# Kernel tuning notes

Hardware: AMD Instinct MI355X
Metric: run time of the kernel (lower is better)

Reference implementation:

```python
import jax, jax.numpy as jnp
import numpy as np

N = 50000; E = 800000; D_IN = 64; EDGE_D = 1
EMB_H = 128; H = 4; C = 32; HC = H * C; G = 8


def _ln(h, g, b):
    mu = jnp.mean(h, axis=-1, keepdims=True)
    var = jnp.var(h, axis=-1, keepdims=True)
    return (h - mu) * jax.lax.rsqrt(var + 1e-5) * g + b


def _tconv(x, src, dst, ea, wq, bq, wk, bk, wv, bv, we, ws, bs):
    # PyG TransformerConv (beta=False, root_weight=True, concat=True, dropout=0)
    n = x.shape[0]
    q = (x @ wq + bq).reshape(n, H, C)
    k = (x @ wk + bk).reshape(n, H, C)
    v = (x @ wv + bv).reshape(n, H, C)
    e = (ea @ we).reshape(-1, H, C)          # [E,H,C] edge embedding (no bias)
    ke = k[src] + e
    ve = v[src] + e
    logit = jnp.einsum('ehc,ehc->eh', q[dst], ke) / np.float32(np.sqrt(C))
    m = jax.ops.segment_max(logit, dst, num_segments=n)
    m = jnp.where(jnp.isfinite(m), m, 0.0)
    a = jnp.exp(logit - m[dst])
    s = jax.ops.segment_sum(a, dst, num_segments=n)
    alpha = a / (s[dst] + 1e-16)             # softmax over in-edges of each dst
    out = jax.ops.segment_sum(alpha[..., None] * ve, dst, num_segments=n)
    out = out.reshape(n, HC)                 # concat heads
    return out + x @ ws + bs                 # root/skip connection


def _embed(x, src, dst, ea, w1, b1, lng, lnb, w2, b2):
    # EmbedConv: per-edge MLP on [x_j || edge_attr], sum-aggregate to dst.
    # LayerNorm params are SHARED (same nn.LayerNorm instance reused in torch).
    msg = jnp.concatenate([x[src], ea], axis=1) @ w1 + b1
    msg = _ln(jax.nn.relu(msg), lng, lnb)
    msg = _ln(jax.nn.relu(msg @ w2 + b2), lng, lnb)
    return jax.ops.segment_sum(msg, dst, num_segments=x.shape[0])


def _forward(x, edge_attr, params, edge_index, batch_idx):
    src, dst = edge_index[0], edge_index[1]
    h = _embed(x, src, dst, edge_attr, *params[0:6])
    h = jax.nn.relu(_tconv(h, src, dst, edge_attr, *params[6:15]))
    h = jax.nn.relu(_tconv(h, src, dst, edge_attr, *params[15:24]))
    # global mean pool
    s = jax.ops.segment_sum(h, batch_idx, num_segments=G)
    cnt = jax.ops.segment_sum(jnp.ones((h.shape[0],), h.dtype), batch_idx, num_segments=G)
    return s / jnp.maximum(cnt, 1.0)[:, None]


def setup_inputs() -> dict:
    key = jax.random.key(0)
    ks = jax.random.split(key, 40)
    w = lambda k, shp: jax.random.normal(k, shp, dtype=jnp.float32) * 0.05
    inp = {}
    inp['x'] = jax.random.normal(ks[0], (N, D_IN), dtype=jnp.float32)
    inp['edge_index'] = jax.random.randint(ks[1], (2, E), 0, N)
    inp['edge_attr'] = jax.random.uniform(ks[2], (E, EDGE_D), dtype=jnp.float32)
    inp['batch_idx'] = jnp.sort(jax.random.randint(ks[3], (N,), 0, G))
    inp['emb_lin1_w'] = w(ks[4], (D_IN + EDGE_D, EMB_H))
    inp['emb_lin1_b'] = jnp.zeros((EMB_H,), jnp.float32)
    inp['emb_ln_g'] = jnp.ones((EMB_H,), jnp.float32)
    inp['emb_ln_b'] = jnp.zeros((EMB_H,), jnp.float32)
    inp['emb_lin2_w'] = w(ks[5], (EMB_H, EMB_H))
    inp['emb_lin2_b'] = jnp.zeros((EMB_H,), jnp.float32)
    i = 6
    for pre, din in (('g1', EMB_H), ('g2', HC)):
        inp[pre + '_wq'] = w(ks[i], (din, HC)); inp[pre + '_bq'] = jnp.zeros((HC,), jnp.float32)
        inp[pre + '_wk'] = w(ks[i + 1], (din, HC)); inp[pre + '_bk'] = jnp.zeros((HC,), jnp.float32)
        inp[pre + '_wv'] = w(ks[i + 2], (din, HC)); inp[pre + '_bv'] = jnp.zeros((HC,), jnp.float32)
        inp[pre + '_we'] = w(ks[i + 3], (EDGE_D, HC))
        inp[pre + '_ws'] = w(ks[i + 4], (din, HC)); inp[pre + '_bs'] = jnp.zeros((HC,), jnp.float32)
        i += 5
    return inp


def reference(x, edge_index, edge_attr, batch_idx,
              emb_lin1_w, emb_lin1_b, emb_ln_g, emb_ln_b, emb_lin2_w, emb_lin2_b,
              g1_wq, g1_bq, g1_wk, g1_bk, g1_wv, g1_bv, g1_we, g1_ws, g1_bs,
              g2_wq, g2_bq, g2_wk, g2_bk, g2_wv, g2_bv, g2_we, g2_ws, g2_bs):
    params = (emb_lin1_w, emb_lin1_b, emb_ln_g, emb_ln_b, emb_lin2_w, emb_lin2_b,
              g1_wq, g1_bq, g1_wk, g1_bk, g1_wv, g1_bv, g1_we, g1_ws, g1_bs,
              g2_wq, g2_bq, g2_wk, g2_bk, g2_wv, g2_bv, g2_we, g2_ws, g2_bs)
    return _forward(x, edge_attr, params, edge_index, batch_idx)
```

## Files before the change

kernel.cpp:

```cpp
#include <hip/hip_runtime.h>

typedef unsigned short u16;
typedef unsigned int u32;
typedef __attribute__((ext_vector_type(8))) short bf16x8;
typedef __attribute__((ext_vector_type(4))) float f32x4;
typedef __attribute__((ext_vector_type(4))) u32 u32x4;

#define N_NODES 50000
#define N_EDGES 800000

__device__ __forceinline__ float bf2f(u16 u) {
    union { u32 i; float f; } v; v.i = ((u32)u) << 16; return v.f;
}
__device__ __forceinline__ u16 f2bf(float f) {
    union { u32 i; float f; } v; v.f = f;
    u32 i = v.i;
    return (u16)((i + 0x7FFFu + ((i >> 16) & 1u)) >> 16);
}
__device__ __forceinline__ float ldf(const void* p, int i, int fl) {
    return fl ? ((const float*)p)[i] : bf2f(((const u16*)p)[i]);
}
__device__ __forceinline__ int getflag(const int* flag) {
    return __builtin_amdgcn_readfirstlane(*flag);
}

struct P8 { const void* s[8]; };

__global__ __launch_bounds__(256) void k_deg_detect(
    const int* __restrict__ dst, int* __restrict__ cnt,
    const u16* __restrict__ xr, int* __restrict__ flag)
{
    int t = threadIdx.x;
    if (blockIdx.x < 3125) {
        int e = blockIdx.x * 256 + t;
        atomicAdd(&cnt[dst[e]], 1);
        return;
    }
    __shared__ int sc[256];
    int c = 0;
    for (int i = t; i < 4096; i += 256) {
        u32 e = (xr[i] >> 7) & 0xFF;
        if (e >= 143) c++;
    }
    sc[t] = c;
    __syncthreads();
    for (int s = 128; s > 0; s >>= 1) {
        if (t < s) sc[t] += sc[t + s];
        __syncthreads();
    }
    if (t == 0) *flag = (sc[0] > 64) ? 1 : 0;
}

__global__ __launch_bounds__(256) void k_prep_all(
    P8 pw, P8 pb, u16* __restrict__ wcat1, u16* __restrict__ wcat2,
    float* __restrict__ bcat1, float* __restrict__ bcat2,
    const void* __restrict__ w2, const void* __restrict__ lng_,
    const void* __restrict__ lnb_, const void* __restrict__ b2_,
    const void* __restrict__ w1, u16* __restrict__ gt,
    float* __restrict__ csum, float* __restrict__ bwp,
    u32* __restrict__ w1pk, const int* __restrict__ flag)
{
    int fl = getflag(flag);
    int b = blockIdx.x, t = threadIdx.x;
    if (b < 512) {
        int gid = b * 256 + t;
        int wi = gid >> 14;
        int id = gid & 16383;
        int k = id >> 7, n = id & 127;
        u16* d = (wi < 4) ? (wcat1 + wi * 16384) : (wcat2 + (wi - 4) * 16384);
        d[n * 128 + k] = f2bf(ldf(pw.s[wi], id, fl));
    } else if (b < 516) {
        int tt = (b - 512) * 256 + t;
        float v = ldf(pb.s[tt >> 7], tt & 127, fl);
        if (tt < 512) bcat1[tt] = v; else bcat2[tt - 512] = v;
    } else {
        if (t < 128) {
            float cs = 0.f, bw = 0.f;
            for (int f = 0; f < 128; f++) {
                float wv = ldf(w2, f * 128 + t, fl);
                float g = ldf(lng_, f, fl);
                float bb = ldf(lnb_, f, fl);
                u16 gwq = f2bf(g * wv);
                gt[t * 128 + f] = gwq;
                cs += bf2f(gwq);
                bw = fmaf(bb, wv, bw);
            }
            csum[t] = cs;
            bwp[t] = bw + ldf(b2_, t, fl);
            if (t < 64)
                w1pk[t] = (u32)f2bf(ldf(w1, 64 * 128 + t * 2, fl)) |
                          ((u32)f2bf(ldf(w1, 64 * 128 + t * 2 + 1, fl)) << 16);
        }
    }
}

__global__ __launch_bounds__(1024) void k_scan(const int* __restrict__ cnt,
                                               int* __restrict__ row_start,
                                               int* __restrict__ nxt)
{
    __shared__ int wsum[16];
    __shared__ int s_tot;
    int t = threadIdx.x, lane = t & 63, wid = t >> 6;
    int run = 0;
    for (int base = 0; base < N_NODES; base += 8192) {
        int i0 = base + t * 8;
        int v[8], pre[8];
        int s = 0;
        #pragma unroll
        for (int j = 0; j < 8; j++) {
            int i = i0 + j;
            v[j] = (i < N_NODES) ? cnt[i] : 0;
            pre[j] = s;
            s += v[j];
        }
        int tsum = s;
        int sc = tsum;
        #pragma unroll
        for (int off = 1; off < 64; off <<= 1) {
            int o = __shfl_up(sc, off);
            if (lane >= off) sc += o;
        }
        if (lane == 63) wsum[wid] = sc;
        __syncthreads();
        if (t == 0) {
            int acc2 = 0;
            #pragma unroll
            for (int k2 = 0; k2 < 16; k2++) { int vv = wsum[k2]; wsum[k2] = acc2; acc2 += vv; }
            s_tot = acc2;
        }
        __syncthreads();
        int texcl = run + wsum[wid] + (sc - tsum);
        #pragma unroll
        for (int j = 0; j < 8; j++) {
            int i = i0 + j;
            if (i < N_NODES) { int ex = texcl + pre[j]; row_start[i] = ex; nxt[i] = ex; }
        }
        run += s_tot;
        __syncthreads();
    }
    if (t == 0) row_start[N_NODES] = run;
}

__global__ __launch_bounds__(256) void k_lin1_scatter(
    const void* __restrict__ x, const void* __restrict__ w1,
    const void* __restrict__ b1, u16* __restrict__ y,
    const int* __restrict__ dst, const int* __restrict__ srcp,
    const void* __restrict__ ea, int* __restrict__ nxt,
    int2* __restrict__ csr, const int* __restrict__ flag)
{
    __shared__ float sx[2][64];
    int fl = getflag(flag);
    int t = threadIdx.x;
    if (blockIdx.x >= 782) {
        int e = (blockIdx.x - 782) * 256 + t;
        if (e < N_EDGES) {
            int p = atomicAdd(&nxt[dst[e]], 1);
            int2 v;
            v.x = srcp[e];
            v.y = __float_as_int(ldf(ea, e, fl));
            csr[p] = v;
        }
        return;
    }
    int col = t & 127, half = t >> 7;
    float wreg[64];
    #pragma unroll
    for (int k = 0; k < 64; k++) wreg[k] = ldf(w1, k * 128 + col, fl);
    float bias = ldf(b1, col, fl);
    int base = blockIdx.x * 64;
    for (int it = 0; it < 32; ++it) {
        __syncthreads();
        if (t < 128) {
            int nh = base + it * 2 + (t >> 6);
            sx[t >> 6][t & 63] = (nh < N_NODES) ? ldf(x, nh * 64 + (t & 63), fl) : 0.f;
        }
        __syncthreads();
        float acc = bias;
        #pragma unroll
        for (int k = 0; k < 64; k++) acc = fmaf(sx[half][k], wreg[k], acc);
        int n = base + it * 2 + half;
        if (n < N_NODES) y[(size_t)n * 128 + col] = f2bf(acc);
    }
}

__global__ __launch_bounds__(256) void k_embed_edges(
    const u16* __restrict__ y, const int2* __restrict__ csr,
    const int* __restrict__ rowst,
    const void* __restrict__ lng, const void* __restrict__ lnb,
    const u16* __restrict__ gt, const u32* __restrict__ w1pk,
    const float* __restrict__ csum, const float* __restrict__ bwp,
    u16* __restrict__ h1, const int* __restrict__ flag)
{
    __shared__ u16 sB[128 * 136];
    __shared__ u32 sW1[64];
    __shared__ float sCSf[128];
    __shared__ float sBWf[128];
    int fl = getflag(flag);
    int t = threadIdx.x;
    for (int c = t; c < 128 * 32; c += 256) {
        int row = c >> 5, ch = c & 31;
        *(ushort4*)&sB[row * 136 + ch * 4] = *(const ushort4*)&gt[row * 128 + ch * 4];
    }
    if (t < 64) sW1[t] = w1pk[t];
    if (t < 128) sCSf[t] = csum[t];
    else sBWf[t - 128] = bwp[t - 128];
    int l = t & 63, w = t >> 6;
    int m = l & 15, q = l >> 4;
    __syncthreads();

    f32x4 zf = {0.f, 0.f, 0.f, 0.f};
    bool sel0 = (m & 1), sel1 = (m & 2), sel2 = (m & 4), sel3 = (m & 8);
    int stride = gridDim.x * 4;
    for (int node = blockIdx.x * 4 + w; node < N_NODES; node += stride) {
        int rs = rowst[node], re = rowst[node + 1];
        float sacc0 = 0.f, sacc1 = 0.f, V = 0.f;
        if (rs < re) {
            int idx = rs + m;
            int2 sa = csr[(idx < re) ? idx : (re - 1)];
            for (int base = rs; base < re; base += 16) {
                float av = __int_as_float(sa.y);
                const u16* yr = y + (size_t)sa.x * 128 + q * 8;
                bf16x8 efrag[4];
                float s1 = 0.f, s2 = 0.f;
                #pragma unroll
                for (int kb = 0; kb < 4; kb++) {
                    u32x4 yu = __builtin_bit_cast(u32x4, *(const bf16x8*)(yr + kb * 32));
                    u32x4 wv4 = *(const u32x4*)&sW1[kb * 16 + q * 4];
                    u32x4 ep;
                    #pragma unroll
                    for (int j2 = 0; j2 < 4; j2++) {
                        u32 yw = yu[j2];
                        u32 ww = wv4[j2];
                        float y0 = __uint_as_float(yw << 16);
                        float y1 = __uint_as_float(yw & 0xffff0000u);
                        float w0 = __uint_as_float(ww << 16);
                        float w1v = __uint_as_float(ww & 0xffff0000u);
                        float u0 = fmaxf(fmaf(av, w0, y0), 0.f);
                        float u1 = fmaxf(fmaf(av, w1v, y1), 0.f);
                        s1 += u0; s2 = fmaf(u0, u0, s2);
                        s1 += u1; s2 = fmaf(u1, u1, s2);
                        ep[j2] = __builtin_amdgcn_perm(__float_as_uint(u1),
                                                       __float_as_uint(u0), 0x07060302u);
                    }
                    efrag[kb] = __builtin_bit_cast(bf16x8, ep);
                }
                int nbase = base + 16;
                if (nbase < re) {
                    int ni = nbase + m;
                    sa = csr[(ni < re) ? ni : (re - 1)];
                }
                s1 += __shfl_xor(s1, 16); s2 += __shfl_xor(s2, 16);
                s1 += __shfl_xor(s1, 32); s2 += __shfl_xor(s2, 32);
                float mu = s1 * (1.f / 128.f);
                float alpha = rsqrtf(s2 * (1.f / 128.f) - mu * mu + 1e-5f);
                float beta = -mu * alpha;

                f32x4 acc[8];
                #pragma unroll
                for (int nb = 0; nb < 8; nb++) acc[nb] = zf;
                #pragma unroll
                for (int nb = 0; nb < 8; nb++) {
                    const u16* grow = &sB[(nb * 16 + m) * 136 + q * 8];
                    #pragma unroll
                    for (int kb = 0; kb < 4; kb++) {
                        bf16x8 gfrag = *(const bf16x8*)(grow + kb * 32);
                        acc[nb] = __builtin_amdgcn_mfma_f32_16x16x32_bf16(gfrag, efrag[kb], acc[nb], 0, 0, 0);
                    }
                }
                float t1 = 0.f, t2 = 0.f;
                #pragma unroll
                for (int nb = 0; nb < 8; nb++) {
                    float4 cs4 = *(const float4*)&sCSf[nb * 16 + q * 4];
                    float4 bw4 = *(const float4*)&sBWf[nb * 16 + q * 4];
                    float csa[4] = {cs4.x, cs4.y, cs4.z, cs4.w};
                    float bwa[4] = {bw4.x, bw4.y, bw4.z, bw4.w};
                    #pragma unroll
                    for (int r = 0; r < 4; r++) {
                        float z = fmaxf(fmaf(alpha, acc[nb][r], fmaf(beta, csa[r], bwa[r])), 0.f);
                        acc[nb][r] = z;
                        t1 += z; t2 = fmaf(z, z, t2);
                    }
                }
                t1 += __shfl_xor(t1, 16); t2 += __shfl_xor(t2, 16);
                t1 += __shfl_xor(t1, 32); t2 += __shfl_xor(t2, 32);
                float mu2 = t1 * (1.f / 128.f);
                float rs2 = rsqrtf(t2 * (1.f / 128.f) - mu2 * mu2 + 1e-5f);
                if (base + m >= re) rs2 = 0.f;
                V = fmaf(rs2, mu2, V);
                float s16v[16];
                #pragma unroll
                for (int k = 0; k < 16; k++) {
                    int nb = k >> 1, rh = (k & 1) << 1;
                    float a = acc[nb][rh] * rs2, b = acc[nb][rh + 1] * rs2;
                    float keep = sel0 ? b : a;
                    float send = sel0 ? a : b;
                    s16v[k] = keep + __shfl_xor(send, 1);
                }
                float s8v[8];
                #pragma unroll
                for (int nb = 0; nb < 8; nb++) {
                    float a = s16v[nb * 2], b = s16v[nb * 2 + 1];
                    float keep = sel1 ? b : a;
                    float send = sel1 ? a : b;
                    s8v[nb] = keep + __shfl_xor(send, 2);
                }
                float s4v[4];
                #pragma unroll
                for (int k = 0; k < 4; k++) {
                    float a = s8v[k * 2], b = s8v[k * 2 + 1];
                    float keep = sel2 ? b : a;
                    float send = sel2 ? a : b;
                    s4v[k] = keep + __shfl_xor(send, 4);
                }
                #pragma unroll
                for (int k = 0; k < 2; k++) {
                    float a = s4v[k * 2], b = s4v[k * 2 + 1];
                    float keep = sel3 ? b : a;
                    float send = sel3 ? a : b;
                    float r2 = keep + __shfl_xor(send, 8);
                    if (k == 0) sacc0 += r2; else sacc1 += r2;
                }
            }
        }
        V += __shfl_xor(V, 1); V += __shfl_xor(V, 2);
        V += __shfl_xor(V, 4); V += __shfl_xor(V, 8);
        float dg = (float)(re - rs);
        #pragma unroll
        for (int k = 0; k < 2; k++) {
            int nb = (k << 2) | (((m >> 3) & 1) << 1) | ((m >> 2) & 1);
            int f = nb * 16 + q * 4 + (m & 3);
            float gg = ldf(lng, f, fl), bb = ldf(lnb, f, fl);
            float sv = (k == 0) ? sacc0 : sacc1;
            h1[(size_t)node * 128 + f] = f2bf(fmaf(gg, sv - V, dg * bb));
        }
    }
}

__global__ __launch_bounds__(256) void k_proj(
    const u16* __restrict__ hin, const u16* __restrict__ wt,
    const float* __restrict__ bcat, u16* __restrict__ outp)
{
    __shared__ u16 sA[64 * 136];
    __shared__ u16 sB[128 * 136];
    int t = threadIdx.x;
    int l = t & 63, w = t >> 6;
    int m = l & 15, q = l >> 4;
    int rowbase = blockIdx.x * 64;
    for (int c = t; c < 64 * 32; c += 256) {
        int row = c >> 5, ch = c & 31;
        int gr = rowbase + row;
        ushort4 pk = make_ushort4(0, 0, 0, 0);
        if (gr < N_NODES) pk = *(const ushort4*)&hin[(size_t)gr * 128 + ch * 4];
        *(ushort4*)&sA[row * 136 + ch * 4] = pk;
    }
    __syncthreads();
    bf16x8 afrag[4];
    #pragma unroll
    for (int kb = 0; kb < 4; kb++)
        afrag[kb] = *(const bf16x8*)&sA[(w * 16 + m) * 136 + kb * 32 + q * 8];

    f32x4 zf = {0.f, 0.f, 0.f, 0.f};
    for (int g = 0; g < 4; ++g) {
        __syncthreads();
        for (int c = t; c < 128 * 32; c += 256) {
            int row = c >> 5, ch = c & 31;
            *(ushort4*)&sB[row * 136 + ch * 4] = *(const ushort4*)&wt[(g * 128 + row) * 128 + ch * 4];
        }
        __syncthreads();
        f32x4 acc[8];
        #pragma unroll
        for (int nb = 0; nb < 8; nb++) acc[nb] = zf;
        #pragma unroll
        for (int nb = 0; nb < 8; nb++) {
            const u16* brow = &sB[(nb * 16 + m) * 136 + q * 8];
            #pragma unroll
            for (int kb = 0; kb < 4; kb++) {
                bf16x8 bfrag = *(const bf16x8*)(brow + kb * 32);
                acc[nb] = __builtin_amdgcn_mfma_f32_16x16x32_bf16(afrag[kb], bfrag, acc[nb], 0, 0, 0);
            }
        }
        #pragma unroll
        for (int nb = 0; nb < 8; nb++) {
            int col = g * 128 + nb * 16 + m;
            float bb = bcat[col];
            #pragma unroll
            for (int r = 0; r < 4; r++) {
                int row = rowbase + w * 16 + q * 4 + r;
                if (row < N_NODES) outp[(size_t)row * 512 + col] = f2bf(acc[nb][r] + bb);
            }
        }
    }
}

__global__ __launch_bounds__(256) void k_attn(
    const u16* __restrict__ qkvs,
    const int* __restrict__ rowst, const int2* __restrict__ csr,
    const void* __restrict__ wep, u16* __restrict__ hout,
    const int* __restrict__ flag)
{
    int fl = getflag(flag);
    int t = threadIdx.x;
    int l = t & 63, w = t >> 6;
    int dstn = blockIdx.x * 4 + w;
    int lane16 = l & 15, sub = l >> 4;
    int f0 = lane16 * 8;
    const float scale = 0.17677669529663687f;

    bf16x8 q8 = *(const bf16x8*)&qkvs[(size_t)dstn * 512 + f0];
    float qf[8], wef[8];
    if (fl) {
        float4 w0 = *(const float4*)((const float*)wep + f0);
        float4 w1v = *(const float4*)((const float*)wep + f0 + 4);
        wef[0] = w0.x; wef[1] = w0.y; wef[2] = w0.z; wef[3] = w0.w;
        wef[4] = w1v.x; wef[5] = w1v.y; wef[6] = w1v.z; wef[7] = w1v.w;
    } else {
        bf16x8 w8 = *(const bf16x8*)((const u16*)wep + f0);
        #pragma unroll
        for (int j = 0; j < 8; j++) wef[j] = bf2f((u16)w8[j]);
    }
    #pragma unroll
    for (int j = 0; j < 8; j++) qf[j] = bf2f((u16)q8[j]) * scale;

    float si = 0.f;
    float a8[8];
    #pragma unroll
    for (int j = 0; j < 8; j++) a8[j] = 0.f;

    int rs = rowst[dstn], re = rowst[dstn + 1];
    int i = rs + sub;
    for (; i + 4 < re; i += 8) {
        int2 sa = csr[i];
        int2 sb = csr[i + 4];
        float ava = __int_as_float(sa.y);
        float avb = __int_as_float(sb.y);
        const u16* sra = &qkvs[(size_t)sa.x * 512 + f0];
        const u16* srb = &qkvs[(size_t)sb.x * 512 + f0];
        bf16x8 k8a = *(const bf16x8*)(sra + 128);
        bf16x8 v8a = *(const bf16x8*)(sra + 256);
        bf16x8 k8b = *(const bf16x8*)(srb + 128);
        bf16x8 v8b = *(const bf16x8*)(srb + 256);
        float pa = 0.f, pb = 0.f;
        float vea[8], veb[8];
        #pragma unroll
        for (int j = 0; j < 8; j++) {
            pa = fmaf(qf[j], fmaf(ava, wef[j], bf2f((u16)k8a[j])), pa);
            pb = fmaf(qf[j], fmaf(avb, wef[j], bf2f((u16)k8b[j])), pb);
            vea[j] = fmaf(ava, wef[j], bf2f((u16)v8a[j]));
            veb[j] = fmaf(avb, wef[j], bf2f((u16)v8b[j]));
        }
        pa += __shfl_xor(pa, 1); pb += __shfl_xor(pb, 1);
        pa += __shfl_xor(pa, 2); pb += __shfl_xor(pb, 2);
        float pea = __expf(pa);
        float peb = __expf(pb);
        si += pea + peb;
        #pragma unroll
        for (int j = 0; j < 8; j++)
            a8[j] = fmaf(pea, vea[j], fmaf(peb, veb[j], a8[j]));
    }
    if (i < re) {
        int2 sa = csr[i];
        float av = __int_as_float(sa.y);
        const u16* sr = &qkvs[(size_t)sa.x * 512 + f0];
        bf16x8 k8 = *(const bf16x8*)(sr + 128);
        bf16x8 v8 = *(const bf16x8*)(sr + 256);
        float p = 0.f;
        float ve[8];
        #pragma unroll
        for (int j = 0; j < 8; j++) {
            p = fmaf(qf[j], fmaf(av, wef[j], bf2f((u16)k8[j])), p);
            ve[j] = fmaf(av, wef[j], bf2f((u16)v8[j]));
        }
        p += __shfl_xor(p, 1); p += __shfl_xor(p, 2);
        float pe = __expf(p);
        si += pe;
        #pragma unroll
        for (int j = 0; j < 8; j++) a8[j] = fmaf(pe, ve[j], a8[j]);
    }
    #pragma unroll
    for (int off = 16; off < 64; off <<= 1) {
        si += __shfl_xor(si, off);
        #pragma unroll
        for (int j = 0; j < 8; j++) a8[j] += __shfl_xor(a8[j], off);
    }
    if (sub == 0) {
        float inv = 1.f / (si + 1e-16f);
        bf16x8 s8 = *(const bf16x8*)&qkvs[(size_t)dstn * 512 + 384 + f0];
        ushort4 p0, p1;
        float o[8];
        #pragma unroll
        for (int j = 0; j < 8; j++)
            o[j] = fmaxf(fmaf(a8[j], inv, bf2f((u16)s8[j])), 0.f);
        p0.x = f2bf(o[0]); p0.y = f2bf(o[1]); p0.z = f2bf(o[2]); p0.w = f2bf(o[3]);
        p1.x = f2bf(o[4]); p1.y = f2bf(o[5]); p1.z = f2bf(o[6]); p1.w = f2bf(o[7]);
        u16* hr = hout + (size_t)dstn * 128 + f0;
        *(ushort4*)hr = p0;
        *(ushort4*)(hr + 4) = p1;
    }
}

__global__ __launch_bounds__(256) void k_pool(
    const u16* __restrict__ h, const int* __restrict__ batch,
    float* __restrict__ gsum, float* __restrict__ gcnt)
{
    __shared__ float ssum[8 * 128];
    __shared__ float scnt[8];
    int t = threadIdx.x;
    for (int i = t; i < 8 * 128; i += 256) ssum[i] = 0.f;
    if (t < 8) scnt[t] = 0.f;
    __syncthreads();
    int f2 = (t & 63) * 2, quarter = t >> 6;
    int per = (N_NODES + gridDim.x - 1) / gridDim.x;
    int lo = blockIdx.x * per;
    int hi = lo + per; if (hi > N_NODES) hi = N_NODES;
    float r0 = 0.f, r1 = 0.f, rcnt = 0.f; int rg = -1;
    for (int n = lo + quarter; n < hi; n += 4) {
        int g = batch[n];
        if (g != rg) {
            if (rg >= 0) {
                atomicAdd(&ssum[rg * 128 + f2], r0);
                atomicAdd(&ssum[rg * 128 + f2 + 1], r1);
                if (f2 == 0) atomicAdd(&scnt[rg], rcnt);
            }
            rg = g; r0 = 0.f; r1 = 0.f; rcnt = 0.f;
        }
        u32 hv = *(const u32*)&h[(size_t)n * 128 + f2];
        r0 += bf2f((u16)(hv & 0xffff));
        r1 += bf2f((u16)(hv >> 16));
        rcnt += 1.f;
    }
    if (rg >= 0) {
        atomicAdd(&ssum[rg * 128 + f2], r0);
        atomicAdd(&ssum[rg * 128 + f2 + 1], r1);
        if (f2 == 0) atomicAdd(&scnt[rg], rcnt);
    }
    __syncthreads();
    for (int i = t; i < 8 * 128; i += 256) unsafeAtomicAdd(&gsum[i], ssum[i]);
    if (t < 8) unsafeAtomicAdd(&gcnt[t], scnt[t]);
}

__global__ void k_out(const float* __restrict__ gsum, const float* __restrict__ gcnt,
                      void* __restrict__ outp, const int* __restrict__ flag) {
    int fl = getflag(flag);
    int t = threadIdx.x;
    float c = fmaxf(gcnt[t >> 7], 1.f);
    float v = gsum[t] / c;
    if (fl) ((float*)outp)[t] = v;
    else ((u16*)outp)[t] = f2bf(v);
}

extern "C" void kernel_launch(void* const* d_in, const int* in_sizes, int n_in,
                              void* d_out, int out_size, void* d_ws, size_t ws_size,
                              hipStream_t stream)
{
    (void)in_sizes; (void)n_in; (void)out_size; (void)ws_size;
    const void* x    = d_in[0];
    const int* ei    = (const int*)d_in[1];
    const void* ea   = d_in[2];
    const int* batch = (const int*)d_in[3];
    const void* w1   = d_in[4];
    const void* b1   = d_in[5];
    const void* lng  = d_in[6];
    const void* lnb  = d_in[7];
    const void* w2   = d_in[8];
    const void* b2   = d_in[9];
    const int* srcp = ei;
    const int* dstp = ei + N_EDGES;

    char* wsb = (char*)d_ws;
    size_t cur = 0;
    auto alloc = [&](size_t sz) -> void* {
        void* p = wsb + cur;
        cur += (sz + 255) & ~(size_t)255;
        return p;
    };
    u16*   y      = (u16*)  alloc((size_t)N_NODES * 128 * 2);
    u16*   h1     = (u16*)  alloc((size_t)N_NODES * 128 * 2);
    u16*   h2     = (u16*)  alloc((size_t)N_NODES * 128 * 2);
    u16*   qkvs   = (u16*)  alloc((size_t)N_NODES * 512 * 2);
    int2*  csr    = (int2*) alloc((size_t)N_EDGES * 8);
    u16*   gt     = (u16*)  alloc(128 * 128 * 2);
    u16*   wcat1  = (u16*)  alloc(512 * 128 * 2);
    u16*   wcat2  = (u16*)  alloc(512 * 128 * 2);
    float* csum   = (float*)alloc(128 * 4);
    float* bwp    = (float*)alloc(128 * 4);
    u32*   w1pk   = (u32*)  alloc(64 * 4);
    float* bcat1  = (float*)alloc(512 * 4);
    float* bcat2  = (float*)alloc(512 * 4);
    int*   cntdeg = (int*)  alloc((size_t)N_NODES * 4);
    int*   rowst  = (int*)  alloc((size_t)(N_NODES + 1) * 4);
    int*   nxt    = (int*)  alloc((size_t)N_NODES * 4);
    float* gsum   = (float*)alloc((8 * 128 + 8) * 4);
    int*   dtflag = (int*)  alloc(256);
    u16*   h3 = h1;

    hipMemsetAsync(cntdeg, 0, (size_t)N_NODES * 4, stream);
    hipMemsetAsync(gsum, 0, (8 * 128 + 8) * 4, stream);

    P8 pw; P8 pb;
    pw.s[0] = d_in[10]; pw.s[1] = d_in[12]; pw.s[2] = d_in[14]; pw.s[3] = d_in[17];
    pw.s[4] = d_in[19]; pw.s[5] = d_in[21]; pw.s[6] = d_in[23]; pw.s[7] = d_in[26];
    pb.s[0] = d_in[11]; pb.s[1] = d_in[13]; pb.s[2] = d_in[15]; pb.s[3] = d_in[18];
    pb.s[4] = d_in[20]; pb.s[5] = d_in[22]; pb.s[6] = d_in[24]; pb.s[7] = d_in[27];

    k_deg_detect<<<3126, 256, 0, stream>>>(dstp, cntdeg, (const u16*)x, dtflag);
    k_prep_all<<<517, 256, 0, stream>>>(pw, pb, wcat1, wcat2, bcat1, bcat2,
                                        w2, lng, lnb, b2, w1, gt, csum, bwp, w1pk, dtflag);
    k_scan<<<1, 1024, 0, stream>>>(cntdeg, rowst, nxt);
    k_lin1_scatter<<<3907, 256, 0, stream>>>(x, w1, b1, y, dstp, srcp, ea, nxt, csr, dtflag);
    k_embed_edges<<<2048, 256, 0, stream>>>(y, csr, rowst, lng, lnb,
                                            gt, w1pk, csum, bwp, h1, dtflag);
    k_proj<<<782, 256, 0, stream>>>(h1, wcat1, bcat1, qkvs);
    k_attn<<<12500, 256, 0, stream>>>(qkvs, rowst, csr, d_in[16], h2, dtflag);
    k_proj<<<782, 256, 0, stream>>>(h2, wcat2, bcat2, qkvs);
    k_attn<<<12500, 256, 0, stream>>>(qkvs, rowst, csr, d_in[25], h3, dtflag);
    k_pool<<<128, 256, 0, stream>>>(h3, batch, gsum, gsum + 8 * 128);
    k_out<<<1, 1024, 0, stream>>>(gsum, gsum + 8 * 128, d_out, dtflag);
}
```

Before: 828.0 us.

## Process two destination nodes per wavefront in embed kernel for ILP

The edge-embedding aggregation kernel now handles a pair of adjacent nodes per wavefront and interleaves their gathers, LayerNorm statistics, MFMA chains and shuffle reductions. All gather loads for both nodes are issued before the math, and the next CSR entries are prefetched. The aim is more independent work in flight to hide gather latency and MFMA dependency stalls. In exchange it doubles register pressure, which may lower occupancy, and a node pair with uneven degrees pays for the larger one, wasting lanes.

```diff
diff --git a/kernel.cpp b/kernel.cpp
--- a/kernel.cpp
+++ b/kernel.cpp
@@ -211,63 +211,98 @@
     f32x4 zf = {0.f, 0.f, 0.f, 0.f};
     bool sel0 = (m & 1), sel1 = (m & 2), sel2 = (m & 4), sel3 = (m & 8);
     int stride = gridDim.x * 4;
-    for (int node = blockIdx.x * 4 + w; node < N_NODES; node += stride) {
-        int rs = rowst[node], re = rowst[node + 1];
-        float sacc0 = 0.f, sacc1 = 0.f, V = 0.f;
-        if (rs < re) {
-            int idx = rs + m;
-            int2 sa = csr[(idx < re) ? idx : (re - 1)];
-            for (int base = rs; base < re; base += 16) {
-                float av = __int_as_float(sa.y);
-                const u16* yr = y + (size_t)sa.x * 128 + q * 8;
-                bf16x8 efrag[4];
-                float s1 = 0.f, s2 = 0.f;
+    const int NPAIR = N_NODES / 2;
+    for (int pid = blockIdx.x * 4 + w; pid < NPAIR; pid += stride) {
+        int n0 = pid * 2, n1 = n0 + 1;
+        int rs0 = rowst[n0];
+        int re0 = rowst[n0 + 1];
+        int re1 = rowst[n0 + 2];
+        int rs1 = re0;
+        int d0 = re0 - rs0, d1 = re1 - rs1;
+        int steps = max((d0 + 15) >> 4, (d1 + 15) >> 4);
+        float sacc0_0 = 0.f, sacc1_0 = 0.f, V0 = 0.f;
+        float sacc0_1 = 0.f, sacc1_1 = 0.f, V1 = 0.f;
+        if (steps > 0) {
+            int lim0 = max(re0 - 1, 0);
+            int lim1 = max(re1 - 1, 0);
+            int2 sa0 = csr[min(rs0 + m, lim0)];
+            int2 sa1 = csr[min(rs1 + m, lim1)];
+            for (int s = 0; s < steps; ++s) {
+                int base0 = rs0 + s * 16, base1 = rs1 + s * 16;
+                float av0 = __int_as_float(sa0.y);
+                float av1 = __int_as_float(sa1.y);
+                const u16* yr0 = y + (size_t)sa0.x * 128 + q * 8;
+                const u16* yr1 = y + (size_t)sa1.x * 128 + q * 8;
+                u32x4 yu0[4], yu1[4];
                 #pragma unroll
                 for (int kb = 0; kb < 4; kb++) {
-                    u32x4 yu = __builtin_bit_cast(u32x4, *(const bf16x8*)(yr + kb * 32));
+                    yu0[kb] = __builtin_bit_cast(u32x4, *(const bf16x8*)(yr0 + kb * 32));
+                    yu1[kb] = __builtin_bit_cast(u32x4, *(const bf16x8*)(yr1 + kb * 32));
+                }
+                int2 sn0 = sa0, sn1 = sa1;
+                if (s + 1 < steps) {
+                    int off = (s + 1) * 16 + m;
+                    sn0 = csr[min(rs0 + off, lim0)];
+                    sn1 = csr[min(rs1 + off, lim1)];
+                }
+                bf16x8 efrag0[4], efrag1[4];
+                float s1_0 = 0.f, s2_0 = 0.f, s1_1 = 0.f, s2_1 = 0.f;
+                #pragma unroll
+                for (int kb = 0; kb < 4; kb++) {
                     u32x4 wv4 = *(const u32x4*)&sW1[kb * 16 + q * 4];
-                    u32x4 ep;
+                    u32x4 ep0, ep1;
                     #pragma unroll
                     for (int j2 = 0; j2 < 4; j2++) {
-                        u32 yw = yu[j2];
                         u32 ww = wv4[j2];
-                        float y0 = __uint_as_float(yw << 16);
-                        float y1 = __uint_as_float(yw & 0xffff0000u);
                         float w0 = __uint_as_float(ww << 16);
                         float w1v = __uint_as_float(ww & 0xffff0000u);
-                        float u0 = fmaxf(fmaf(av, w0, y0), 0.f);
-                        float u1 = fmaxf(fmaf(av, w1v, y1), 0.f);
-                        s1 += u0; s2 = fmaf(u0, u0, s2);
-                        s1 += u1; s2 = fmaf(u1, u1, s2);
-                        ep[j2] = __builtin_amdgcn_perm(__float_as_uint(u1),
-                                                       __float_as_uint(u0), 0x07060302u);
+                        u32 ya = yu0[kb][j2];
+                        u32 yb = yu1[kb][j2];
+                        float ya0 = __uint_as_float(ya << 16);
+                        float ya1 = __uint_as_float(ya & 0xffff0000u);
+                        float yb0 = __uint_as_float(yb << 16);
+                        float yb1 = __uint_as_float(yb & 0xffff0000u);
+                        float ua0 = fmaxf(fmaf(av0, w0, ya0), 0.f);
+                        float ua1 = fmaxf(fmaf(av0, w1v, ya1), 0.f);
+                        float ub0 = fmaxf(fmaf(av1, w0, yb0), 0.f);
+                        float ub1 = fmaxf(fmaf(av1, w1v, yb1), 0.f);
+                        s1_0 += ua0; s2_0 = fmaf(ua0, ua0, s2_0);
+                        s1_0 += ua1; s2_0 = fmaf(ua1, ua1, s2_0);
+                        s1_1 += ub0; s2_1 = fmaf(ub0, ub0, s2_1);
+                        s1_1 += ub1; s2_1 = fmaf(ub1, ub1, s2_1);
+                        ep0[j2] = __builtin_amdgcn_perm(__float_as_uint(ua1),
+                                                        __float_as_uint(ua0), 0x07060302u);
+                        ep1[j2] = __builtin_amdgcn_perm(__float_as_uint(ub1),
+                                                        __float_as_uint(ub0), 0x07060302u);
                     }
-                    efrag[kb] = __builtin_bit_cast(bf16x8, ep);
-                }
-                int nbase = base + 16;
-                if (nbase < re) {
-                    int ni = nbase + m;
-                    sa = csr[(ni < re) ? ni : (re - 1)];
-                }
-                s1 += __shfl_xor(s1, 16); s2 += __shfl_xor(s2, 16);
-                s1 += __shfl_xor(s1, 32); s2 += __shfl_xor(s2, 32);
-                float mu = s1 * (1.f / 128.f);
-                float alpha = rsqrtf(s2 * (1.f / 128.f) - mu * mu + 1e-5f);
-                float beta = -mu * alpha;
-
-                f32x4 acc[8];
-                #pragma unroll
-                for (int nb = 0; nb < 8; nb++) acc[nb] = zf;
+                    efrag0[kb] = __builtin_bit_cast(bf16x8, ep0);
+                    efrag1[kb] = __builtin_bit_cast(bf16x8, ep1);
+                }
+                s1_0 += __shfl_xor(s1_0, 16); s1_1 += __shfl_xor(s1_1, 16);
+                s2_0 += __shfl_xor(s2_0, 16); s2_1 += __shfl_xor(s2_1, 16);
+                s1_0 += __shfl_xor(s1_0, 32); s1_1 += __shfl_xor(s1_1, 32);
+                s2_0 += __shfl_xor(s2_0, 32); s2_1 += __shfl_xor(s2_1, 32);
+                float mu_0 = s1_0 * (1.f / 128.f);
+                float alpha0 = rsqrtf(s2_0 * (1.f / 128.f) - mu_0 * mu_0 + 1e-5f);
+                float beta0 = -mu_0 * alpha0;
+                float mu_1 = s1_1 * (1.f / 128.f);
+                float alpha1 = rsqrtf(s2_1 * (1.f / 128.f) - mu_1 * mu_1 + 1e-5f);
+                float beta1 = -mu_1 * alpha1;
+
+                f32x4 acc0[8], acc1[8];
+                #pragma unroll
+                for (int nb = 0; nb < 8; nb++) { acc0[nb] = zf; acc1[nb] = zf; }
                 #pragma unroll
                 for (int nb = 0; nb < 8; nb++) {
                     const u16* grow = &sB[(nb * 16 + m) * 136 + q * 8];
                     #pragma unroll
                     for (int kb = 0; kb < 4; kb++) {
                         bf16x8 gfrag = *(const bf16x8*)(grow + kb * 32);
-                        acc[nb] = __builtin_amdgcn_mfma_f32_16x16x32_bf16(gfrag, efrag[kb], acc[nb], 0, 0, 0);
+                        acc0[nb] = __builtin_amdgcn_mfma_f32_16x16x32_bf16(gfrag, efrag0[kb], acc0[nb], 0, 0, 0);
+                        acc1[nb] = __builtin_amdgcn_mfma_f32_16x16x32_bf16(gfrag, efrag1[kb], acc1[nb], 0, 0, 0);
                     }
                 }
-                float t1 = 0.f, t2 = 0.f;
+                float t1_0 = 0.f, t2_0 = 0.f, t1_1 = 0.f, t2_1 = 0.f;
                 #pragma unroll
                 for (int nb = 0; nb < 8; nb++) {
                     float4 cs4 = *(const float4*)&sCSf[nb * 16 + q * 4];
@@ -276,62 +311,86 @@
                     float bwa[4] = {bw4.x, bw4.y, bw4.z, bw4.w};
                     #pragma unroll
                     for (int r = 0; r < 4; r++) {
-                        float z = fmaxf(fmaf(alpha, acc[nb][r], fmaf(beta, csa[r], bwa[r])), 0.f);
-                        acc[nb][r] = z;
-                        t1 += z; t2 = fmaf(z, z, t2);
+                        float z0 = fmaxf(fmaf(alpha0, acc0[nb][r], fmaf(beta0, csa[r], bwa[r])), 0.f);
+                        float z1 = fmaxf(fmaf(alpha1, acc1[nb][r], fmaf(beta1, csa[r], bwa[r])), 0.f);
+                        acc0[nb][r] = z0;
+                        acc1[nb][r] = z1;
+                        t1_0 += z0; t2_0 = fmaf(z0, z0, t2_0);
+                        t1_1 += z1; t2_1 = fmaf(z1, z1, t2_1);
                     }
                 }
-                t1 += __shfl_xor(t1, 16); t2 += __shfl_xor(t2, 16);
-                t1 += __shfl_xor(t1, 32); t2 += __shfl_xor(t2, 32);
-                float mu2 = t1 * (1.f / 128.f);
-                float rs2 = rsqrtf(t2 * (1.f / 128.f) - mu2 * mu2 + 1e-5f);
-                if (base + m >= re) rs2 = 0.f;
-                V = fmaf(rs2, mu2, V);
-                float s16v[16];
+                t1_0 += __shfl_xor(t1_0, 16); t1_1 += __shfl_xor(t1_1, 16);
+                t2_0 += __shfl_xor(t2_0, 16); t2_1 += __shfl_xor(t2_1, 16);
+                t1_0 += __shfl_xor(t1_0, 32); t1_1 += __shfl_xor(t1_1, 32);
+                t2_0 += __shfl_xor(t2_0, 32); t2_1 += __shfl_xor(t2_1, 32);
+                float mu2_0 = t1_0 * (1.f / 128.f);
+                float rs2_0 = rsqrtf(t2_0 * (1.f / 128.f) - mu2_0 * mu2_0 + 1e-5f);
+                float mu2_1 = t1_1 * (1.f / 128.f);
+                float rs2_1 = rsqrtf(t2_1 * (1.f / 128.f) - mu2_1 * mu2_1 + 1e-5f);
+                if (base0 + m >= re0) rs2_0 = 0.f;
+                if (base1 + m >= re1) rs2_1 = 0.f;
+                V0 = fmaf(rs2_0, mu2_0, V0);
+                V1 = fmaf(rs2_1, mu2_1, V1);
+                float s16v_0[16], s16v_1[16];
                 #pragma unroll
                 for (int k = 0; k < 16; k++) {
                     int nb = k >> 1, rh = (k & 1) << 1;
-                    float a = acc[nb][rh] * rs2, b = acc[nb][rh + 1] * rs2;
-                    float keep = sel0 ? b : a;
-                    float send = sel0 ? a : b;
-                    s16v[k] = keep + __shfl_xor(send, 1);
-                }
-                float s8v[8];
+                    float a0 = acc0[nb][rh] * rs2_0, b0 = acc0[nb][rh + 1] * rs2_0;
+                    float a1 = acc1[nb][rh] * rs2_1, b1 = acc1[nb][rh + 1] * rs2_1;
+                    float keep0 = sel0 ? b0 : a0, send0 = sel0 ? a0 : b0;
+                    float keep1 = sel0 ? b1 : a1, send1 = sel0 ? a1 : b1;
+                    s16v_0[k] = keep0 + __shfl_xor(send0, 1);
+                    s16v_1[k] = keep1 + __shfl_xor(send1, 1);
+                }
+                float s8v_0[8], s8v_1[8];
                 #pragma unroll
                 for (int nb = 0; nb < 8; nb++) {
-                    float a = s16v[nb * 2], b = s16v[nb * 2 + 1];
-                    float keep = sel1 ? b : a;
-                    float send = sel1 ? a : b;
-                    s8v[nb] = keep + __shfl_xor(send, 2);
-                }
-                float s4v[4];
+                    float a0 = s16v_0[nb * 2], b0 = s16v_0[nb * 2 + 1];
+                    float a1 = s16v_1[nb * 2], b1 = s16v_1[nb * 2 + 1];
+                    float keep0 = sel1 ? b0 : a0, send0 = sel1 ? a0 : b0;
+                    float keep1 = sel1 ? b1 : a1, send1 = sel1 ? a1 : b1;
+                    s8v_0[nb] = keep0 + __shfl_xor(send0, 2);
+                    s8v_1[nb] = keep1 + __shfl_xor(send1, 2);
+                }
+                float s4v_0[4], s4v_1[4];
                 #pragma unroll
                 for (int k = 0; k < 4; k++) {
-                    float a = s8v[k * 2], b = s8v[k * 2 + 1];
-                    float keep = sel2 ? b : a;
-                    float send = sel2 ? a : b;
-                    s4v[k] = keep + __shfl_xor(send, 4);
+                    float a0 = s8v_0[k * 2], b0 = s8v_0[k * 2 + 1];
+                    float a1 = s8v_1[k * 2], b1 = s8v_1[k * 2 + 1];
+                    float keep0 = sel2 ? b0 : a0, send0 = sel2 ? a0 : b0;
+                    float keep1 = sel2 ? b1 : a1, send1 = sel2 ? a1 : b1;
+                    s4v_0[k] = keep0 + __shfl_xor(send0, 4);
+                    s4v_1[k] = keep1 + __shfl_xor(send1, 4);
                 }
                 #pragma unroll
                 for (int k = 0; k < 2; k++) {
-                    float a = s4v[k * 2], b = s4v[k * 2 + 1];
-                    float keep = sel3 ? b : a;
-                    float send = sel3 ? a : b;
-                    float r2 = keep + __shfl_xor(send, 8);
-                    if (k == 0) sacc0 += r2; else sacc1 += r2;
-                }
+                    float a0 = s4v_0[k * 2], b0 = s4v_0[k * 2 + 1];
+                    float a1 = s4v_1[k * 2], b1 = s4v_1[k * 2 + 1];
+                    float keep0 = sel3 ? b0 : a0, send0 = sel3 ? a0 : b0;
+                    float keep1 = sel3 ? b1 : a1, send1 = sel3 ? a1 : b1;
+                    float r20 = keep0 + __shfl_xor(send0, 8);
+                    float r21 = keep1 + __shfl_xor(send1, 8);
+                    if (k == 0) { sacc0_0 += r20; sacc0_1 += r21; }
+                    else        { sacc1_0 += r20; sacc1_1 += r21; }
+                }
+                sa0 = sn0;
+                sa1 = sn1;
             }
         }
-        V += __shfl_xor(V, 1); V += __shfl_xor(V, 2);
-        V += __shfl_xor(V, 4); V += __shfl_xor(V, 8);
-        float dg = (float)(re - rs);
+        V0 += __shfl_xor(V0, 1); V1 += __shfl_xor(V1, 1);
+        V0 += __shfl_xor(V0, 2); V1 += __shfl_xor(V1, 2);
+        V0 += __shfl_xor(V0, 4); V1 += __shfl_xor(V1, 4);
+        V0 += __shfl_xor(V0, 8); V1 += __shfl_xor(V1, 8);
+        float dg0 = (float)d0, dg1 = (float)d1;
         #pragma unroll
         for (int k = 0; k < 2; k++) {
             int nb = (k << 2) | (((m >> 3) & 1) << 1) | ((m >> 2) & 1);
             int f = nb * 16 + q * 4 + (m & 3);
             float gg = ldf(lng, f, fl), bb = ldf(lnb, f, fl);
-            float sv = (k == 0) ? sacc0 : sacc1;
-            h1[(size_t)node * 128 + f] = f2bf(fmaf(gg, sv - V, dg * bb));
+            float sv0 = (k == 0) ? sacc0_0 : sacc1_0;
+            float sv1 = (k == 0) ? sacc0_1 : sacc1_1;
+            h1[(size_t)n0 * 128 + f] = f2bf(fmaf(gg, sv0 - V0, dg0 * bb));
+            h1[(size_t)n1 * 128 + f] = f2bf(fmaf(gg, sv1 - V1, dg1 * bb));
         }
     }
 }
```

After: 810.6 us. 2.1% less time.

## Split embed edge work into 16-edge groups with atomic fp32 accumulation

Applied to the files above, without the earlier changes.

Replaces the grid-strided per-node edge-embedding kernel with one wave per 16-edge group, built from a second prefix scan and a group-list kernel. Partial sums are atomically added into a zeroed fp32 staging buffer, and a new finalize kernel applies the shared LayerNorm affine and converts to bf16. This targets load imbalance from varying node degrees and exposes more parallelism, at the cost of two extra launches, a large memset, fp32 atomics and extra staging-buffer traffic.

```diff
diff --git a/kernel.cpp b/kernel.cpp
--- a/kernel.cpp
+++ b/kernel.cpp
@@ -8,6 +8,7 @@
 
 #define N_NODES 50000
 #define N_EDGES 800000
+#define NG_MAX ((N_EDGES + 15 * N_NODES) / 16)
 
 __device__ __forceinline__ float bf2f(u16 u) {
     union { u32 i; float f; } v; v.i = ((u32)u) << 16; return v.f;
@@ -96,49 +97,73 @@
 
 __global__ __launch_bounds__(1024) void k_scan(const int* __restrict__ cnt,
                                                int* __restrict__ row_start,
-                                               int* __restrict__ nxt)
+                                               int* __restrict__ nxt,
+                                               int* __restrict__ gstart)
 {
     __shared__ int wsum[16];
-    __shared__ int s_tot;
+    __shared__ int wsum2[16];
+    __shared__ int s_tot, s_tot2;
     int t = threadIdx.x, lane = t & 63, wid = t >> 6;
-    int run = 0;
+    int run = 0, run2 = 0;
     for (int base = 0; base < N_NODES; base += 8192) {
         int i0 = base + t * 8;
-        int v[8], pre[8];
-        int s = 0;
+        int v[8], pre[8], gpre[8];
+        int s = 0, gs = 0;
         #pragma unroll
         for (int j = 0; j < 8; j++) {
             int i = i0 + j;
             v[j] = (i < N_NODES) ? cnt[i] : 0;
-            pre[j] = s;
-            s += v[j];
-        }
-        int tsum = s;
-        int sc = tsum;
+            pre[j] = s;  s += v[j];
+            gpre[j] = gs; gs += (v[j] + 15) >> 4;
+        }
+        int tsum = s, gsum = gs;
+        int sc = tsum, sc2 = gsum;
         #pragma unroll
         for (int off = 1; off < 64; off <<= 1) {
             int o = __shfl_up(sc, off);
-            if (lane >= off) sc += o;
-        }
-        if (lane == 63) wsum[wid] = sc;
+            int o2 = __shfl_up(sc2, off);
+            if (lane >= off) { sc += o; sc2 += o2; }
+        }
+        if (lane == 63) { wsum[wid] = sc; wsum2[wid] = sc2; }
         __syncthreads();
         if (t == 0) {
-            int acc2 = 0;
+            int acc2 = 0, acc3 = 0;
             #pragma unroll
-            for (int k2 = 0; k2 < 16; k2++) { int vv = wsum[k2]; wsum[k2] = acc2; acc2 += vv; }
-            s_tot = acc2;
+            for (int k2 = 0; k2 < 16; k2++) {
+                int vv = wsum[k2]; wsum[k2] = acc2; acc2 += vv;
+                int v2 = wsum2[k2]; wsum2[k2] = acc3; acc3 += v2;
+            }
+            s_tot = acc2; s_tot2 = acc3;
         }
         __syncthreads();
         int texcl = run + wsum[wid] + (sc - tsum);
+        int gexcl = run2 + wsum2[wid] + (sc2 - gsum);
         #pragma unroll
         for (int j = 0; j < 8; j++) {
             int i = i0 + j;
-            if (i < N_NODES) { int ex = texcl + pre[j]; row_start[i] = ex; nxt[i] = ex; }
-        }
-        run += s_tot;
-        __syncthreads();
-    }
-    if (t == 0) row_start[N_NODES] = run;
+            if (i < N_NODES) {
+                int ex = texcl + pre[j];
+                row_start[i] = ex; nxt[i] = ex;
+                gstart[i] = gexcl + gpre[j];
+            }
+        }
+        run += s_tot; run2 += s_tot2;
+        __syncthreads();
+    }
+    if (t == 0) { row_start[N_NODES] = run; gstart[N_NODES] = run2; }
+}
+
+__global__ __launch_bounds__(256) void k_glist(
+    const int* __restrict__ rowst, const int* __restrict__ gstart,
+    int2* __restrict__ glist)
+{
+    int n = blockIdx.x * 256 + threadIdx.x;
+    if (n >= N_NODES) return;
+    int rs = rowst[n], re = rowst[n + 1];
+    int gs = gstart[n];
+    int cnt = (re - rs + 15) >> 4;
+    for (int k = 0; k < cnt; k++)
+        glist[gs + k] = make_int2(n, rs + k * 16);
 }
 
 __global__ __launch_bounds__(256) void k_lin1_scatter(
@@ -183,19 +208,18 @@
     }
 }
 
-__global__ __launch_bounds__(256) void k_embed_edges(
+__global__ __launch_bounds__(256) void k_embed_grp(
     const u16* __restrict__ y, const int2* __restrict__ csr,
-    const int* __restrict__ rowst,
-    const void* __restrict__ lng, const void* __restrict__ lnb,
+    const int* __restrict__ rowst, const int* __restrict__ gstart,
+    const int2* __restrict__ glist,
     const u16* __restrict__ gt, const u32* __restrict__ w1pk,
     const float* __restrict__ csum, const float* __restrict__ bwp,
-    u16* __restrict__ h1, const int* __restrict__ flag)
+    float* __restrict__ h1stage, float* __restrict__ vacc)
 {
     __shared__ u16 sB[128 * 136];
     __shared__ u32 sW1[64];
     __shared__ float sCSf[128];
     __shared__ float sBWf[128];
-    int fl = getflag(flag);
     int t = threadIdx.x;
     for (int c = t; c < 128 * 32; c += 256) {
         int row = c >> 5, ch = c & 31;
@@ -207,133 +231,148 @@
     int l = t & 63, w = t >> 6;
     int m = l & 15, q = l >> 4;
     __syncthreads();
+    int ng = gstart[N_NODES];
+    int gid = blockIdx.x * 4 + w;
+    if (gid >= ng) return;
+    int2 ge = glist[gid];
+    int node = ge.x, base = ge.y;
+    int re = rowst[node + 1];
+    int row = base + m;
+    if (row >= re) row = re - 1;
+    int2 sa = csr[row];
+    float av = __int_as_float(sa.y);
+    const u16* yr = y + (size_t)sa.x * 128 + q * 8;
+
+    bf16x8 efrag[4];
+    float s1 = 0.f, s2 = 0.f;
+    #pragma unroll
+    for (int kb = 0; kb < 4; kb++) {
+        u32x4 yu = __builtin_bit_cast(u32x4, *(const bf16x8*)(yr + kb * 32));
+        u32x4 wv4 = *(const u32x4*)&sW1[kb * 16 + q * 4];
+        u32x4 ep;
+        #pragma unroll
+        for (int j2 = 0; j2 < 4; j2++) {
+            u32 yw = yu[j2];
+            u32 ww = wv4[j2];
+            float y0 = __uint_as_float(yw << 16);
+            float y1 = __uint_as_float(yw & 0xffff0000u);
+            float w0 = __uint_as_float(ww << 16);
+            float w1v = __uint_as_float(ww & 0xffff0000u);
+            float u0 = fmaxf(fmaf(av, w0, y0), 0.f);
+            float u1 = fmaxf(fmaf(av, w1v, y1), 0.f);
+            s1 += u0; s2 = fmaf(u0, u0, s2);
+            s1 += u1; s2 = fmaf(u1, u1, s2);
+            ep[j2] = __builtin_amdgcn_perm(__float_as_uint(u1),
+                                           __float_as_uint(u0), 0x07060302u);
+        }
+        efrag[kb] = __builtin_bit_cast(bf16x8, ep);
+    }
+    s1 += __shfl_xor(s1, 16); s2 += __shfl_xor(s2, 16);
+    s1 += __shfl_xor(s1, 32); s2 += __shfl_xor(s2, 32);
+    float mu = s1 * (1.f / 128.f);
+    float alpha = rsqrtf(s2 * (1.f / 128.f) - mu * mu + 1e-5f);
+    float beta = -mu * alpha;
 
     f32x4 zf = {0.f, 0.f, 0.f, 0.f};
+    f32x4 acc[8];
+    #pragma unroll
+    for (int nb = 0; nb < 8; nb++) acc[nb] = zf;
+    #pragma unroll
+    for (int nb = 0; nb < 8; nb++) {
+        const u16* grow = &sB[(nb * 16 + m) * 136 + q * 8];
+        #pragma unroll
+        for (int kb = 0; kb < 4; kb++) {
+            bf16x8 gfrag = *(const bf16x8*)(grow + kb * 32);
+            acc[nb] = __builtin_amdgcn_mfma_f32_16x16x32_bf16(gfrag, efrag[kb], acc[nb], 0, 0, 0);
+        }
+    }
+    float t1 = 0.f, t2 = 0.f;
+    #pragma unroll
+    for (int nb = 0; nb < 8; nb++) {
+        float4 cs4 = *(const float4*)&sCSf[nb * 16 + q * 4];
+        float4 bw4 = *(const float4*)&sBWf[nb * 16 + q * 4];
+        float csa[4] = {cs4.x, cs4.y, cs4.z, cs4.w};
+        float bwa[4] = {bw4.x, bw4.y, bw4.z, bw4.w};
+        #pragma unroll
+        for (int r = 0; r < 4; r++) {
+            float z = fmaxf(fmaf(alpha, acc[nb][r], fmaf(beta, csa[r], bwa[r])), 0.f);
+            acc[nb][r] = z;
+            t1 += z; t2 = fmaf(z, z, t2);
+        }
+    }
+    t1 += __shfl_xor(t1, 16); t2 += __shfl_xor(t2, 16);
+    t1 += __shfl_xor(t1, 32); t2 += __shfl_xor(t2, 32);
+    float mu2 = t1 * (1.f / 128.f);
+    float rs2 = rsqrtf(t2 * (1.f / 128.f) - mu2 * mu2 + 1e-5f);
+    if (base + m >= re) rs2 = 0.f;
+    float Vc = rs2 * mu2;
+
     bool sel0 = (m & 1), sel1 = (m & 2), sel2 = (m & 4), sel3 = (m & 8);
-    int stride = gridDim.x * 4;
-    for (int node = blockIdx.x * 4 + w; node < N_NODES; node += stride) {
-        int rs = rowst[node], re = rowst[node + 1];
-        float sacc0 = 0.f, sacc1 = 0.f, V = 0.f;
-        if (rs < re) {
-            int idx = rs + m;
-            int2 sa = csr[(idx < re) ? idx : (re - 1)];
-            for (int base = rs; base < re; base += 16) {
-                float av = __int_as_float(sa.y);
-                const u16* yr = y + (size_t)sa.x * 128 + q * 8;
-                bf16x8 efrag[4];
-                float s1 = 0.f, s2 = 0.f;
-                #pragma unroll
-                for (int kb = 0; kb < 4; kb++) {
-                    u32x4 yu = __builtin_bit_cast(u32x4, *(const bf16x8*)(yr + kb * 32));
-                    u32x4 wv4 = *(const u32x4*)&sW1[kb * 16 + q * 4];
-                    u32x4 ep;
-                    #pragma unroll
-                    for (int j2 = 0; j2 < 4; j2++) {
-                        u32 yw = yu[j2];
-                        u32 ww = wv4[j2];
-                        float y0 = __uint_as_float(yw << 16);
-                        float y1 = __uint_as_float(yw & 0xffff0000u);
-                        float w0 = __uint_as_float(ww << 16);
-                        float w1v = __uint_as_float(ww & 0xffff0000u);
-                        float u0 = fmaxf(fmaf(av, w0, y0), 0.f);
-                        float u1 = fmaxf(fmaf(av, w1v, y1), 0.f);
-                        s1 += u0; s2 = fmaf(u0, u0, s2);
-                        s1 += u1; s2 = fmaf(u1, u1, s2);
-                        ep[j2] = __builtin_amdgcn_perm(__float_as_uint(u1),
-                                                       __float_as_uint(u0), 0x07060302u);
-                    }
-                    efrag[kb] = __builtin_bit_cast(bf16x8, ep);
-                }
-                int nbase = base + 16;
-                if (nbase < re) {
-                    int ni = nbase + m;
-                    sa = csr[(ni < re) ? ni : (re - 1)];
-                }
-                s1 += __shfl_xor(s1, 16); s2 += __shfl_xor(s2, 16);
-                s1 += __shfl_xor(s1, 32); s2 += __shfl_xor(s2, 32);
-                float mu = s1 * (1.f / 128.f);
-                float alpha = rsqrtf(s2 * (1.f / 128.f) - mu * mu + 1e-5f);
-                float beta = -mu * alpha;
-
-                f32x4 acc[8];
-                #pragma unroll
-                for (int nb = 0; nb < 8; nb++) acc[nb] = zf;
-                #pragma unroll
-                for (int nb = 0; nb < 8; nb++) {
-                    const u16* grow = &sB[(nb * 16 + m) * 136 + q * 8];
-                    #pragma unroll
-                    for (int kb = 0; kb < 4; kb++) {
-                        bf16x8 gfrag = *(const bf16x8*)(grow + kb * 32);
-                        acc[nb] = __builtin_amdgcn_mfma_f32_16x16x32_bf16(gfrag, efrag[kb], acc[nb], 0, 0, 0);
-                    }
-                }
-                float t1 = 0.f, t2 = 0.f;
-                #pragma unroll
-                for (int nb = 0; nb < 8; nb++) {
-                    float4 cs4 = *(const float4*)&sCSf[nb * 16 + q * 4];
-                    float4 bw4 = *(const float4*)&sBWf[nb * 16 + q * 4];
-                    float csa[4] = {cs4.x, cs4.y, cs4.z, cs4.w};
-                    float bwa[4] = {bw4.x, bw4.y, bw4.z, bw4.w};
-                    #pragma unroll
-                    for (int r = 0; r < 4; r++) {
-                        float z = fmaxf(fmaf(alpha, acc[nb][r], fmaf(beta, csa[r], bwa[r])), 0.f);
-                        acc[nb][r] = z;
-                        t1 += z; t2 = fmaf(z, z, t2);
-                    }
-                }
-                t1 += __shfl_xor(t1, 16); t2 += __shfl_xor(t2, 16);
-                t1 += __shfl_xor(t1, 32); t2 += __shfl_xor(t2, 32);
-                float mu2 = t1 * (1.f / 128.f);
-                float rs2 = rsqrtf(t2 * (1.f / 128.f) - mu2 * mu2 + 1e-5f);
-                if (base + m >= re) rs2 = 0.f;
-                V = fmaf(rs2, mu2, V);
-                float s16v[16];
-                #pragma unroll
-                for (int k = 0; k < 16; k++) {
-                    int nb = k >> 1, rh = (k & 1) << 1;
-                    float a = acc[nb][rh] * rs2, b = acc[nb][rh + 1] * rs2;
-                    float keep = sel0 ? b : a;
-                    float send = sel0 ? a : b;
-                    s16v[k] = keep + __shfl_xor(send, 1);
-                }
-                float s8v[8];
-                #pragma unroll
-                for (int nb = 0; nb < 8; nb++) {
-                    float a = s16v[nb * 2], b = s16v[nb * 2 + 1];
-                    float keep = sel1 ? b : a;
-                    float send = sel1 ? a : b;
-                    s8v[nb] = keep + __shfl_xor(send, 2);
-                }
-                float s4v[4];
-                #pragma unroll
-                for (int k = 0; k < 4; k++) {
-                    float a = s8v[k * 2], b = s8v[k * 2 + 1];
-                    float keep = sel2 ? b : a;
-                    float send = sel2 ? a : b;
-                    s4v[k] = keep + __shfl_xor(send, 4);
-                }
-                #pragma unroll
-                for (int k = 0; k < 2; k++) {
-                    float a = s4v[k * 2], b = s4v[k * 2 + 1];
-                    float keep = sel3 ? b : a;
-                    float send = sel3 ? a : b;
-                    float r2 = keep + __shfl_xor(send, 8);
-                    if (k == 0) sacc0 += r2; else sacc1 += r2;
-                }
-            }
-        }
-        V += __shfl_xor(V, 1); V += __shfl_xor(V, 2);
-        V += __shfl_xor(V, 4); V += __shfl_xor(V, 8);
-        float dg = (float)(re - rs);
-        #pragma unroll
-        for (int k = 0; k < 2; k++) {
-            int nb = (k << 2) | (((m >> 3) & 1) << 1) | ((m >> 2) & 1);
-            int f = nb * 16 + q * 4 + (m & 3);
-            float gg = ldf(lng, f, fl), bb = ldf(lnb, f, fl);
-            float sv = (k == 0) ? sacc0 : sacc1;
-            h1[(size_t)node * 128 + f] = f2bf(fmaf(gg, sv - V, dg * bb));
-        }
-    }
+    float sacc0, sacc1;
+    {
+        float s16v[16];
+        #pragma unroll
+        for (int k = 0; k < 16; k++) {
+            int nb = k >> 1, rh = (k & 1) << 1;
+            float a = acc[nb][rh] * rs2, b = acc[nb][rh + 1] * rs2;
+            float keep = sel0 ? b : a;
+            float send = sel0 ? a : b;
+            s16v[k] = keep + __shfl_xor(send, 1);
+        }
+        float s8v[8];
+        #pragma unroll
+        for (int nb = 0; nb < 8; nb++) {
+            float a = s16v[nb * 2], b = s16v[nb * 2 + 1];
+            float keep = sel1 ? b : a;
+            float send = sel1 ? a : b;
+            s8v[nb] = keep + __shfl_xor(send, 2);
+        }
+        float s4v[4];
+        #pragma unroll
+        for (int k = 0; k < 4; k++) {
+            float a = s8v[k * 2], b = s8v[k * 2 + 1];
+            float keep = sel2 ? b : a;
+            float send = sel2 ? a : b;
+            s4v[k] = keep + __shfl_xor(send, 4);
+        }
+        float a0 = s4v[0], b0 = s4v[1];
+        float keep0 = sel3 ? b0 : a0, send0 = sel3 ? a0 : b0;
+        sacc0 = keep0 + __shfl_xor(send0, 8);
+        float a1 = s4v[2], b1 = s4v[3];
+        float keep1 = sel3 ? b1 : a1, send1 = sel3 ? a1 : b1;
+        sacc1 = keep1 + __shfl_xor(send1, 8);
+    }
+    Vc += __shfl_xor(Vc, 1); Vc += __shfl_xor(Vc, 2);
+    Vc += __shfl_xor(Vc, 4); Vc += __shfl_xor(Vc, 8);
+    if (l == 0) unsafeAtomicAdd(&vacc[node], Vc);
+    #pragma unroll
+    for (int k = 0; k < 2; k++) {
+        int nb = (k << 2) | (((m >> 3) & 1) << 1) | ((m >> 2) & 1);
+        int f = nb * 16 + q * 4 + (m & 3);
+        float sv = (k == 0) ? sacc0 : sacc1;
+        unsafeAtomicAdd(&h1stage[(size_t)node * 128 + f], sv);
+    }
+}
+
+__global__ __launch_bounds__(256) void k_embed_fin(
+    const float* __restrict__ h1stage, const float* __restrict__ vacc,
+    const int* __restrict__ rowst,
+    const void* __restrict__ lng, const void* __restrict__ lnb,
+    u16* __restrict__ h1, const int* __restrict__ flag)
+{
+    int fl = getflag(flag);
+    int idx = blockIdx.x * 256 + threadIdx.x;
+    int node = idx >> 5;
+    int f4 = (idx & 31) * 4;
+    float4 sv = *(const float4*)&h1stage[(size_t)node * 128 + f4];
+    float V = vacc[node];
+    float dg = (float)(rowst[node + 1] - rowst[node]);
+    ushort4 o;
+    o.x = f2bf(fmaf(ldf(lng, f4 + 0, fl), sv.x - V, dg * ldf(lnb, f4 + 0, fl)));
+    o.y = f2bf(fmaf(ldf(lng, f4 + 1, fl), sv.y - V, dg * ldf(lnb, f4 + 1, fl)));
+    o.z = f2bf(fmaf(ldf(lng, f4 + 2, fl), sv.z - V, dg * ldf(lnb, f4 + 2, fl)));
+    o.w = f2bf(fmaf(ldf(lng, f4 + 3, fl), sv.w - V, dg * ldf(lnb, f4 + 3, fl)));
+    *(ushort4*)&h1[(size_t)node * 128 + f4] = o;
 }
 
 __global__ __launch_bounds__(256) void k_proj(
@@ -591,10 +630,15 @@
     int*   nxt    = (int*)  alloc((size_t)N_NODES * 4);
     float* gsum   = (float*)alloc((8 * 128 + 8) * 4);
     int*   dtflag = (int*)  alloc(256);
+    float* h1stage = (float*)alloc((size_t)N_NODES * 128 * 4);
+    float* vacc    = (float*)alloc((size_t)N_NODES * 4);
+    int*   gstart  = (int*)  alloc((size_t)(N_NODES + 1) * 4);
+    int2*  glist   = (int2*) alloc((size_t)NG_MAX * 8);
     u16*   h3 = h1;
 
     hipMemsetAsync(cntdeg, 0, (size_t)N_NODES * 4, stream);
     hipMemsetAsync(gsum, 0, (8 * 128 + 8) * 4, stream);
+    hipMemsetAsync(h1stage, 0, (size_t)N_NODES * 128 * 4 + 256 + (size_t)N_NODES * 4, stream);
 
     P8 pw; P8 pb;
     pw.s[0] = d_in[10]; pw.s[1] = d_in[12]; pw.s[2] = d_in[14]; pw.s[3] = d_in[17];
@@ -605,10 +649,12 @@
     k_deg_detect<<<3126, 256, 0, stream>>>(dstp, cntdeg, (const u16*)x, dtflag);
     k_prep_all<<<517, 256, 0, stream>>>(pw, pb, wcat1, wcat2, bcat1, bcat2,
                                         w2, lng, lnb, b2, w1, gt, csum, bwp, w1pk, dtflag);
-    k_scan<<<1, 1024, 0, stream>>>(cntdeg, rowst, nxt);
+    k_scan<<<1, 1024, 0, stream>>>(cntdeg, rowst, nxt, gstart);
+    k_glist<<<196, 256, 0, stream>>>(rowst, gstart, glist);
     k_lin1_scatter<<<3907, 256, 0, stream>>>(x, w1, b1, y, dstp, srcp, ea, nxt, csr, dtflag);
-    k_embed_edges<<<2048, 256, 0, stream>>>(y, csr, rowst, lng, lnb,
-                                            gt, w1pk, csum, bwp, h1, dtflag);
+    k_embed_grp<<<(NG_MAX + 3) / 4, 256, 0, stream>>>(y, csr, rowst, gstart, glist,
+                                                      gt, w1pk, csum, bwp, h1stage, vacc);
+    k_embed_fin<<<6250, 256, 0, stream>>>(h1stage, vacc, rowst, lng, lnb, h1, dtflag);
     k_proj<<<782, 256, 0, stream>>>(h1, wcat1, bcat1, qkvs);
     k_attn<<<12500, 256, 0, stream>>>(qkvs, rowst, csr, d_in[16], h2, dtflag);
     k_proj<<<782, 256, 0, stream>>>(h2, wcat2, bcat2, qkvs);
```

Result: faster. 787.0 us (-5.0%).
